# Kernel tuning notes

Measured on AMD Instinct MI355X. Metric: run time of the kernel, lower is better.

The kernel has to match this reference:

```python
import jax, jax.numpy as jnp
import numpy as np

H = 16  # head_num


def setup_inputs() -> dict:
    key = jax.random.key(0)
    ks = jax.random.split(key, 16)
    B, N, D, DR = 4, 512, 1024, 128
    dk = D // H
    nrm = lambda i, shp, sc=1.0: jax.random.normal(ks[i], shp, jnp.float32) * sc
    inp = {
        "q": nrm(0, (B, N, D)),
        "k": nrm(1, (B, N, D)),
        "v": nrm(2, (B, N, D)),
        "r_k": nrm(3, (B, N, N, DR), 0.1),
        "r_v": nrm(4, (B, N, N, DR), 0.1),
        # learned params (Linear stored as [in, out] so y = x @ W + b)
        "Wq": nrm(5, (D, D), 1.0 / np.sqrt(D)), "bq": jnp.zeros((D,), jnp.float32),
        "Wk": nrm(6, (D, D), 1.0 / np.sqrt(D)), "bk": jnp.zeros((D,), jnp.float32),
        "Wv": nrm(7, (D, D), 1.0 / np.sqrt(D)), "bv": jnp.zeros((D,), jnp.float32),
        "Wrk": nrm(8, (DR, dk), 1.0 / np.sqrt(DR)), "brk": jnp.zeros((dk,), jnp.float32),
        "Wrv": nrm(9, (DR, dk), 1.0 / np.sqrt(DR)), "brv": jnp.zeros((dk,), jnp.float32),
        "Wo": nrm(10, (D, D), 1.0 / np.sqrt(D)), "bo": jnp.zeros((D,), jnp.float32),
    }
    return inp


def reference(q, k, v, r_k, r_v, Wq, bq, Wk, bk, Wv, bv, Wrk, brk, Wrv, brv, Wo, bo):
    B, N, D = q.shape
    dk = D // H
    scale = 1.0 / np.sqrt(dk).astype(np.float32)
    # relation projections ('concat' mode, rel_share=False): [B,N,N,d_rel] -> [B,N,N,d_k]
    rk = r_k @ Wrk + brk
    rv = r_v @ Wrv + brv

    def heads(x, W, b):  # [B,N,D] -> [B,H,N,dk]
        return (x @ W + b).reshape(B, N, H, dk).transpose(0, 2, 1, 3)

    qh = heads(q, Wq, bq)
    kh = heads(k, Wk, bk)
    vh = heads(v, Wv, bv)
    # score_1: standard scaled dot-product; score_2: relation bias per (query m, key n)
    score = jnp.einsum('bhmd,bhnd->bhmn', qh, kh) * scale \
          + jnp.einsum('bhmd,bmnd->bhmn', qh, rk)
    att = jax.nn.softmax(score, axis=-1)  # [B,H,N,N]
    # value_1: standard AV; value_2: relation-value combination
    val = jnp.einsum('bhmn,bhnd->bhmd', att, vh) \
        + jnp.einsum('bhmn,bmnd->bhmd', att, rv)
    out = val.transpose(0, 2, 1, 3).reshape(B, N, D) @ Wo + bo
    return out
```

## Files before the change

### kernel.cpp

```cpp
#include <hip/hip_runtime.h>
#include <hip/hip_bf16.h>
#include <hip/hip_fp16.h>
#include <stdint.h>


typedef __attribute__((ext_vector_type(4))) float f32x4;
typedef __attribute__((ext_vector_type(8))) short s16x8;

#define MFMA16(A, B, C) __builtin_amdgcn_mfma_f32_16x16x32_bf16(A, B, C, 0, 0, 0)

__device__ __forceinline__ uint16_t f2bf(float x) {
  uint32_t u = __float_as_uint(x);
  u += 0x7fffu + ((u >> 16) & 1u);
  return (uint16_t)(u >> 16);
}
__device__ __forceinline__ float bf2f(uint16_t u) {
  return __uint_as_float((uint32_t)u << 16);
}
__device__ __forceinline__ uint16_t f2h(float x) {
  __half h = __float2half_rn(x);
  return *reinterpret_cast<uint16_t*>(&h);
}
__device__ __forceinline__ float h2f(uint16_t u) {
  __half h = *reinterpret_cast<__half*>(&u);
  return __half2float(h);
}

__device__ __forceinline__ s16x8 pack8(float4 a, float4 b) {
  s16x8 r;
  r[0] = (short)f2bf(a.x); r[1] = (short)f2bf(a.y); r[2] = (short)f2bf(a.z); r[3] = (short)f2bf(a.w);
  r[4] = (short)f2bf(b.x); r[5] = (short)f2bf(b.y); r[6] = (short)f2bf(b.z); r[7] = (short)f2bf(b.w);
  return r;
}

__device__ __forceinline__ void gll16(const void* g, void* l) {
  __builtin_amdgcn_global_load_lds(
      (const __attribute__((address_space(1))) uint32_t*)(g),
      (__attribute__((address_space(3))) uint32_t*)(l), 16, 0, 0);
}

__global__ __launch_bounds__(256) void k_prep(
    const float* __restrict__ Wq, const float* __restrict__ Wk,
    const float* __restrict__ Wv, const float* __restrict__ Wo,
    const float* __restrict__ Wrk, const float* __restrict__ Wrv,
    uint16_t* __restrict__ WqT, uint16_t* __restrict__ WkT,
    uint16_t* __restrict__ WvT, uint16_t* __restrict__ WoT,
    uint16_t* __restrict__ WrkB, uint16_t* __restrict__ WrvT) {
  int z = blockIdx.y;
  int t = threadIdx.x;
  if (z == 4) {
    if (blockIdx.x == 0) {
      for (int i = t; i < 128 * 64; i += 256) WrkB[i] = f2bf(Wrk[i]);
      for (int i = t; i < 64 * 128; i += 256) {
        int d = i >> 7, r = i & 127;
        WrvT[i] = f2bf(Wrv[r * 64 + d]);
      }
    }
    return;
  }
  const float* W = (z == 0) ? Wq : (z == 1) ? Wk : (z == 2) ? Wv : Wo;
  uint16_t* O = (z == 0) ? WqT : (z == 1) ? WkT : (z == 2) ? WvT : WoT;
  int tk = (blockIdx.x >> 4) * 64;
  int tn = (blockIdx.x & 15) * 64;
  __shared__ float tile[64][65];
  {
    int kk = t >> 2, c0 = (t & 3) * 16;
    const float* src = W + (size_t)(tk + kk) * 1024 + tn + c0;
#pragma unroll
    for (int i = 0; i < 16; i += 4) {
      float4 v = *(const float4*)(src + i);
      tile[kk][c0 + i + 0] = v.x; tile[kk][c0 + i + 1] = v.y;
      tile[kk][c0 + i + 2] = v.z; tile[kk][c0 + i + 3] = v.w;
    }
  }
  __syncthreads();
  {
    int n_loc = t >> 2;
    int n = tn + n_loc;
#pragma unroll
    for (int cc = 0; cc < 2; ++cc) {
      int c = (t & 3) * 2 + cc;
      int csrc = c ^ (n & 7);
      s16x8 pk;
#pragma unroll
      for (int j = 0; j < 8; ++j) pk[j] = (short)f2bf(tile[csrc * 8 + j][n_loc]);
      *reinterpret_cast<s16x8*>(O + (size_t)n * 1024 + tk + c * 8) = pk;
    }
  }
}

__global__ __launch_bounds__(256) void k_projqkv(
    const float* __restrict__ Xq, const float* __restrict__ Xk,
    const float* __restrict__ Xv, const uint16_t* __restrict__ WTbase,
    const float* __restrict__ bq, const float* __restrict__ bk,
    const float* __restrict__ bv, uint16_t* __restrict__ outbase) {
  int mode = blockIdx.z;
  const float* X = (mode == 0) ? Xq : (mode == 1) ? Xk : Xv;
  const float* bias = (mode == 0) ? bq : (mode == 1) ? bk : bv;
  const uint16_t* WT = WTbase + (size_t)mode * (1u << 20);
  uint16_t* out = outbase + (size_t)mode * (2u << 20);

  __shared__ alignas(16) uint16_t As[128 * 64];
  __shared__ alignas(16) uint16_t Bs[128 * 64];
  int t = threadIdx.x, lane = t & 63, w = t >> 6, lr = lane & 15, lg = lane >> 4;
  int m0 = blockIdx.x * 128, n0 = blockIdx.y * 128;
  int wm = (w >> 1) * 64, wn = (w & 1) * 64;
  f32x4 acc[4][4];
#pragma unroll
  for (int i = 0; i < 4; ++i)
#pragma unroll
    for (int j = 0; j < 4; ++j) acc[i][j] = (f32x4){0.f, 0.f, 0.f, 0.f};
  int srow = t >> 1, sh = t & 1;
  for (int ko = 0; ko < 16; ++ko) {
    __syncthreads();
    {
      const float* src = X + (size_t)(m0 + srow) * 1024 + ko * 64 + sh * 32;
#pragma unroll
      for (int c = 0; c < 4; ++c) {
        float4 v0 = *(const float4*)(src + c * 8);
        float4 v1 = *(const float4*)(src + c * 8 + 4);
        s16x8 pk = pack8(v0, v1);
        *reinterpret_cast<s16x8*>((char*)As + srow * 128 +
                                  ((((sh * 4 + c) * 16)) ^ ((srow & 7) << 4))) = pk;
      }
      const uint16_t* bsrc = WT + (size_t)(n0 + srow) * 1024 + ko * 64 + sh * 32;
#pragma unroll
      for (int c = 0; c < 4; ++c) {
        s16x8 vb = *(const s16x8*)(bsrc + c * 8);
        *reinterpret_cast<s16x8*>((char*)Bs + srow * 128 + (sh * 4 + c) * 16) = vb;
      }
    }
    __syncthreads();
#pragma unroll
    for (int kk = 0; kk < 2; ++kk) {
      s16x8 af[4], bf[4];
#pragma unroll
      for (int mt = 0; mt < 4; ++mt) {
        int row = wm + mt * 16 + lr;
        af[mt] = *(const s16x8*)((const char*)As + row * 128 +
                                 (((kk * 32 + lg * 8) * 2) ^ ((row & 7) << 4)));
      }
#pragma unroll
      for (int nt = 0; nt < 4; ++nt) {
        int row = wn + nt * 16 + lr;
        bf[nt] = *(const s16x8*)((const char*)Bs + row * 128 +
                                 (((kk * 32 + lg * 8) * 2) ^ ((row & 7) << 4)));
      }
#pragma unroll
      for (int mt = 0; mt < 4; ++mt)
#pragma unroll
        for (int nt = 0; nt < 4; ++nt)
          acc[mt][nt] = MFMA16(af[mt], bf[nt], acc[mt][nt]);
    }
  }
  float sc = (mode == 1) ? 0.125f : 1.0f;
#pragma unroll
  for (int mt = 0; mt < 4; ++mt) {
#pragma unroll
    for (int nt = 0; nt < 4; ++nt) {
      int col = n0 + wn + nt * 16 + lr;
      float bcol = bias[col];
      if (mode != 2) {
#pragma unroll
        for (int r = 0; r < 4; ++r) {
          int row = m0 + wm + mt * 16 + lg * 4 + r;
          out[(size_t)row * 1024 + col] = f2bf((acc[mt][nt][r] + bcol) * sc);
        }
      } else {
        int row0 = m0 + wm + mt * 16 + lg * 4;
        int b = row0 >> 9, n = row0 & 511;
        int h = col >> 6, d = col & 63;
        ushort4 pk;
        pk.x = f2bf(acc[mt][nt][0] + bcol);
        pk.y = f2bf(acc[mt][nt][1] + bcol);
        pk.z = f2bf(acc[mt][nt][2] + bcol);
        pk.w = f2bf(acc[mt][nt][3] + bcol);
        *reinterpret_cast<ushort4*>(out + ((size_t)(b * 16 + h) * 64 + d) * 512 + n) = pk;
      }
    }
  }
}

__global__ __launch_bounds__(256) void k_qt(
    const uint16_t* __restrict__ qh, const uint16_t* __restrict__ WrkB,
    uint16_t* __restrict__ qt) {
  int t = threadIdx.x, lane = t & 63, w = t >> 6, lr = lane & 15, lg = lane >> 4;
  int row0 = blockIdx.x * 64 + w * 16;
  f32x4 acc[8];
#pragma unroll
  for (int i = 0; i < 8; ++i) acc[i] = (f32x4){0.f, 0.f, 0.f, 0.f};
  s16x8 af[2];
#pragma unroll
  for (int kk = 0; kk < 2; ++kk)
    af[kk] = *(const s16x8*)(qh + (size_t)(row0 + lr) * 64 + kk * 32 + lg * 8);
#pragma unroll
  for (int rt = 0; rt < 8; ++rt) {
#pragma unroll
    for (int kk = 0; kk < 2; ++kk) {
      s16x8 bf = *(const s16x8*)(WrkB + (size_t)(rt * 16 + lr) * 64 + kk * 32 + lg * 8);
      acc[rt] = MFMA16(af[kk], bf, acc[rt]);
    }
  }
#pragma unroll
  for (int rt = 0; rt < 8; ++rt)
#pragma unroll
    for (int r = 0; r < 4; ++r)
      qt[(size_t)(row0 + lg * 4 + r) * 128 + rt * 16 + lr] = f2bf(acc[rt][r]);
}

__global__ __launch_bounds__(256, 2) void k_score1(
    const uint16_t* __restrict__ qh, const uint16_t* __restrict__ kh,
    uint16_t* __restrict__ S1) {
  int t = threadIdx.x, lane = t & 63, w = t >> 6, lr = lane & 15, lg = lane >> 4;
  int mt = blockIdx.x, h = blockIdx.y, b = blockIdx.z;
  int mrow = b * 512 + mt * 64 + w * 16 + lr;
  const uint16_t* qrow = qh + (size_t)mrow * 1024 + h * 64 + lg * 8;
  s16x8 bq0 = *(const s16x8*)(qrow);
  s16x8 bq1 = *(const s16x8*)(qrow + 32);
  const uint16_t* krow = kh + ((size_t)b * 512 + lr) * 1024 + h * 64 + lg * 8;
  f32x4 acc[32];
#pragma unroll
  for (int i = 0; i < 32; ++i) acc[i] = (f32x4){0.f, 0.f, 0.f, 0.f};
#pragma unroll
  for (int g = 0; g < 4; ++g) {
    s16x8 ka[8][2];
#pragma unroll
    for (int i = 0; i < 8; ++i) {
      const uint16_t* p = krow + (size_t)((g * 8 + i) * 16) * 1024;
      ka[i][0] = *(const s16x8*)(p);
      ka[i][1] = *(const s16x8*)(p + 32);
    }
#pragma unroll
    for (int i = 0; i < 8; ++i) {
      acc[g * 8 + i] = MFMA16(ka[i][0], bq0, acc[g * 8 + i]);
      acc[g * 8 + i] = MFMA16(ka[i][1], bq1, acc[g * 8 + i]);
    }
  }
#pragma unroll
  for (int nt = 0; nt < 32; ++nt) {
    int nsw = (nt * 16 + lg * 4) ^ ((h & 7) << 3);
    ushort4 u;
    u.x = f2h(acc[nt][0]); u.y = f2h(acc[nt][1]);
    u.z = f2h(acc[nt][2]); u.w = f2h(acc[nt][3]);
    *(ushort4*)(S1 + (size_t)mrow * 8192 + h * 512 + nsw) = u;
  }
}

#define RKSTEP(s)                                                              \
  {                                                                            \
    asm volatile("s_waitcnt vmcnt(%0)" ::                                      \
                 "i"(((s) <= 27) ? 6 : (31 - (s)) * 2) : "memory");            \
    const char* bp_ = wpriv + ((s) & 3) * 2048 + lr * 128;                     \
    float4 v0_ = *(const float4*)(bp_ + (((lg * 2 + 0) ^ (lr & 7)) * 16));     \
    float4 v1_ = *(const float4*)(bp_ + (((lg * 2 + 1) ^ (lr & 7)) * 16));     \
    acc[(s) >> 2] = MFMA16(aqt[(s) & 3], pack8(v0_, v1_), acc[(s) >> 2]);      \
    if ((s) + 4 < 32) {                                                        \
      const int s2_ = (s) + 4;                                                 \
      const char* src_ = rkb + (size_t)((s2_ >> 2) * 64 + w * 16 + r_lo) * 512 \
                         + (s2_ & 3) * 128 + c16s * 16;                        \
      char* dst_ = wpriv + (s2_ & 3) * 2048 + lane * 16;                       \
      gll16(src_, dst_);                                                       \
      gll16(src_ + 8 * 512, dst_ + 1024);                                      \
    }                                                                          \
  }

__global__ __launch_bounds__(256, 3) void k_s2v2(
    const uint16_t* __restrict__ qt, const float* __restrict__ rk,
    const float* __restrict__ rv, uint16_t* SATT,
    const uint16_t* __restrict__ WrvT, const float* __restrict__ brv,
    uint16_t* __restrict__ V2) {
  int bm = blockIdx.x;
  int t = threadIdx.x, lane = t & 63, w = t >> 6, lr = lane & 15, lg = lane >> 4;
  __shared__ alignas(16) char stream_lds[32768];
  __shared__ alignas(16) uint16_t att_lds[16 * 512];
  __shared__ alignas(16) uint16_t arv_lds[16 * 128];
  __shared__ float red[2][16][4];
  char* wpriv = stream_lds + w * 8192;
  const int r_lo = lane >> 3;
  const int c16s = (lane & 7) ^ r_lo;

  s16x8 aqt[4];
#pragma unroll
  for (int kk = 0; kk < 4; ++kk)
    aqt[kk] = *(const s16x8*)(qt + ((size_t)bm * 16 + lr) * 128 + kk * 32 + lg * 8);
  const char* s1g = (const char*)(SATT + (size_t)bm * 8192);
#pragma unroll
  for (int i = 0; i < 4; ++i)
    gll16(s1g + i * 4096 + t * 16, (char*)att_lds + i * 4096 + t * 16);
  asm volatile("s_waitcnt vmcnt(0)" ::: "memory");

  const char* rkb = (const char*)(rk + (size_t)bm * 65536);
#pragma unroll
  for (int s2 = 0; s2 < 4; ++s2) {
    const char* src_ = rkb + (size_t)((s2 >> 2) * 64 + w * 16 + r_lo) * 512 +
                       (s2 & 3) * 128 + c16s * 16;
    char* dst_ = wpriv + (s2 & 3) * 2048 + lane * 16;
    gll16(src_, dst_);
    gll16(src_ + 8 * 512, dst_ + 1024);
  }

  f32x4 acc[8];
#pragma unroll
  for (int j = 0; j < 8; ++j) acc[j] = (f32x4){0.f, 0.f, 0.f, 0.f};

  RKSTEP(0)  RKSTEP(1)  RKSTEP(2)  RKSTEP(3)  RKSTEP(4)  RKSTEP(5)  RKSTEP(6)  RKSTEP(7)
  RKSTEP(8)  RKSTEP(9)  RKSTEP(10) RKSTEP(11) RKSTEP(12) RKSTEP(13) RKSTEP(14) RKSTEP(15)
  RKSTEP(16) RKSTEP(17) RKSTEP(18) RKSTEP(19) RKSTEP(20) RKSTEP(21) RKSTEP(22) RKSTEP(23)
  RKSTEP(24) RKSTEP(25) RKSTEP(26) RKSTEP(27) RKSTEP(28) RKSTEP(29) RKSTEP(30) RKSTEP(31)

  const char* rvb = (const char*)(rv + (size_t)bm * 65536);
#pragma unroll
  for (int c = 0; c < 2; ++c) {
#pragma unroll
    for (int g = 0; g < 4; ++g) {
      const char* src_ = rvb + (size_t)(c * 32 + g * 8 + r_lo) * 512 + w * 128 +
                         (lane & 7) * 16;
      gll16(src_, wpriv + c * 4096 + g * 1024 + lane * 16);
    }
  }
  __syncthreads();

#pragma unroll
  for (int idx = 0; idx < 8; ++idx) {
#pragma unroll
    for (int r = 0; r < 4; ++r) {
      int h = lg * 4 + r;
      int n = idx * 64 + w * 16 + lr;
      uint16_t s1v = *(const uint16_t*)((const char*)att_lds + h * 1024 +
                     (((uint32_t)n * 2) ^ ((uint32_t)(h & 7) << 4)));
      acc[idx][r] += h2f(s1v);
    }
  }

  float mrow[4], inv[4];
#pragma unroll
  for (int r = 0; r < 4; ++r) {
    float mx = acc[0][r];
#pragma unroll
    for (int j = 1; j < 8; ++j) mx = fmaxf(mx, acc[j][r]);
#pragma unroll
    for (int off = 1; off < 16; off <<= 1) mx = fmaxf(mx, __shfl_xor(mx, off, 64));
    mrow[r] = mx;
  }
  if (lr == 0) {
#pragma unroll
    for (int r = 0; r < 4; ++r) red[0][lg * 4 + r][w] = mrow[r];
  }
  __syncthreads();
#pragma unroll
  for (int r = 0; r < 4; ++r) {
    const float* p = red[0][lg * 4 + r];
    mrow[r] = fmaxf(fmaxf(p[0], p[1]), fmaxf(p[2], p[3]));
  }
#pragma unroll
  for (int r = 0; r < 4; ++r) {
    float s = 0.f;
#pragma unroll
    for (int j = 0; j < 8; ++j) {
      float pj = __expf(acc[j][r] - mrow[r]);
      acc[j][r] = pj;
      s += pj;
    }
#pragma unroll
    for (int off = 1; off < 16; off <<= 1) s += __shfl_xor(s, off, 64);
    inv[r] = s;
  }
  if (lr == 0) {
#pragma unroll
    for (int r = 0; r < 4; ++r) red[1][lg * 4 + r][w] = inv[r];
  }
  __syncthreads();
#pragma unroll
  for (int r = 0; r < 4; ++r) {
    const float* p = red[1][lg * 4 + r];
    inv[r] = 1.f / (p[0] + p[1] + p[2] + p[3]);
  }
#pragma unroll
  for (int r = 0; r < 4; ++r) {
    int h = lg * 4 + r;
#pragma unroll
    for (int idx = 0; idx < 8; ++idx) {
      int n = idx * 64 + w * 16 + lr;
      uint32_t off = (uint32_t)h * 1024 + (((uint32_t)n * 2) ^ ((uint32_t)(h & 7) << 4));
      *(uint16_t*)((char*)att_lds + off) = f2bf(acc[idx][r] * inv[r]);
    }
  }
  __syncthreads();

#pragma unroll
  for (int i = 0; i < 4; ++i) {
    s16x8 vv = *(const s16x8*)((const char*)att_lds + i * 4096 + t * 16);
    *(s16x8*)((char*)SATT + (size_t)bm * 16384 + i * 4096 + t * 16) = vv;
  }
  asm volatile("" ::: "memory");

  f32x4 arv0 = (f32x4){0.f, 0.f, 0.f, 0.f}, arv1 = arv0;
#define RV_CONSUME(c)                                                          \
  {                                                                            \
    s16x8 a_ = *(const s16x8*)((const char*)att_lds + lr * 1024 +              \
               (((uint32_t)((c) * 64 + lg * 16)) ^ ((uint32_t)(lr & 7) << 4)));\
    const float* vb_ = (const float*)(wpriv + ((c) & 1) * 4096);               \
    s16x8 bf0_, bf1_;                                                          \
    _Pragma("unroll")                                                          \
    for (int i = 0; i < 8; ++i) bf0_[i] = (short)f2bf(vb_[(lg * 8 + i) * 32 + lr]); \
    _Pragma("unroll")                                                          \
    for (int i = 0; i < 8; ++i) bf1_[i] = (short)f2bf(vb_[(lg * 8 + i) * 32 + 16 + lr]); \
    arv0 = MFMA16(a_, bf0_, arv0);                                             \
    arv1 = MFMA16(a_, bf1_, arv1);                                             \
  }
#pragma unroll 1
  for (int c = 0; c < 14; ++c) {
    asm volatile("s_waitcnt vmcnt(4)" ::: "memory");
    RV_CONSUME(c)
#pragma unroll
    for (int g = 0; g < 4; ++g) {
      const char* src_ = rvb + (size_t)((c + 2) * 32 + g * 8 + r_lo) * 512 + w * 128 +
                         (lane & 7) * 16;
      gll16(src_, wpriv + ((c + 2) & 1) * 4096 + g * 1024 + lane * 16);
    }
  }
  asm volatile("s_waitcnt vmcnt(4)" ::: "memory");
  RV_CONSUME(14)
  asm volatile("s_waitcnt vmcnt(0)" ::: "memory");
  RV_CONSUME(15)

#pragma unroll
  for (int r = 0; r < 4; ++r) {
    int h = lg * 4 + r;
    uint32_t rc0 = (uint32_t)(w * 32 + lr) * 2;
    uint32_t rc1 = (uint32_t)(w * 32 + 16 + lr) * 2;
    *(uint16_t*)((char*)arv_lds + h * 256 + (rc0 ^ ((uint32_t)(h & 7) << 4))) = f2bf(arv0[r]);
    *(uint16_t*)((char*)arv_lds + h * 256 + (rc1 ^ ((uint32_t)(h & 7) << 4))) = f2bf(arv1[r]);
  }
  __syncthreads();
  f32x4 vacc = (f32x4){0.f, 0.f, 0.f, 0.f};
#pragma unroll
  for (int kk = 0; kk < 4; ++kk) {
    uint32_t rb = (uint32_t)(kk * 32 + lg * 8) * 2;
    s16x8 a = *(const s16x8*)((const char*)arv_lds + lr * 256 +
                              (rb ^ ((uint32_t)(lr & 7) << 4)));
    s16x8 bfw = *(const s16x8*)(WrvT + (size_t)(w * 16 + lr) * 128 + kk * 32 + lg * 8);
    vacc = MFMA16(a, bfw, vacc);
  }
  float bias = brv[w * 16 + lr];
#pragma unroll
  for (int r = 0; r < 4; ++r)
    V2[(size_t)bm * 1024 + (lg * 4 + r) * 64 + w * 16 + lr] = f2bf(vacc[r] + bias);
}

__global__ __launch_bounds__(256) void k_val1(
    const uint16_t* __restrict__ vhT, const uint16_t* __restrict__ ATT,
    const uint16_t* __restrict__ V2, uint16_t* __restrict__ VALB) {
  int t = threadIdx.x, lane = t & 63, w = t >> 6, lr = lane & 15, lg = lane >> 4;
  int mt = blockIdx.x, h = blockIdx.y, b = blockIdx.z;
  int mb = mt * 64 + w * 16;
  const uint16_t* vrow = vhT + ((size_t)((b * 16 + h) * 64) + lr) * 512 + lg * 8;
  const uint16_t* arow = ATT + (size_t)(b * 512 + mb + lr) * 8192 + h * 512;
  f32x4 acc[4];
#pragma unroll
  for (int j = 0; j < 4; ++j) acc[j] = (f32x4){0.f, 0.f, 0.f, 0.f};
#pragma unroll 4
  for (int kk = 0; kk < 16; ++kk) {
    int nsw = (kk * 32 + lg * 8) ^ ((h & 7) << 3);
    s16x8 a0 = *(const s16x8*)(arow + nsw);
#pragma unroll
    for (int dt = 0; dt < 4; ++dt) {
      s16x8 vf = *(const s16x8*)(vrow + (size_t)dt * 16 * 512 + kk * 32);
      acc[dt] = MFMA16(vf, a0, acc[dt]);
    }
  }
#pragma unroll
  for (int dt = 0; dt < 4; ++dt) {
    size_t adr = (size_t)(b * 512 + mb + lr) * 1024 + h * 64 + dt * 16 + lg * 4;
    ushort4 v2v = *(const ushort4*)(V2 + adr);
    ushort4 o;
    o.x = f2bf(acc[dt][0] + bf2f(v2v.x));
    o.y = f2bf(acc[dt][1] + bf2f(v2v.y));
    o.z = f2bf(acc[dt][2] + bf2f(v2v.z));
    o.w = f2bf(acc[dt][3] + bf2f(v2v.w));
    *(ushort4*)(VALB + adr) = o;
  }
}

__global__ __launch_bounds__(256) void k_out(
    const uint16_t* __restrict__ A, const uint16_t* __restrict__ WT,
    const float* __restrict__ bias, float* __restrict__ out) {
  __shared__ alignas(16) uint16_t As[128 * 64];
  __shared__ alignas(16) uint16_t Bs[128 * 64];
  int t = threadIdx.x, lane = t & 63, w = t >> 6, lr = lane & 15, lg = lane >> 4;
  int m0 = blockIdx.x * 128, n0 = blockIdx.y * 128;
  int wm = (w >> 1) * 64, wn = (w & 1) * 64;
  f32x4 acc[4][4];
#pragma unroll
  for (int i = 0; i < 4; ++i)
#pragma unroll
    for (int j = 0; j < 4; ++j) acc[i][j] = (f32x4){0.f, 0.f, 0.f, 0.f};
  int srow = t >> 1, sh = t & 1;
  for (int ko = 0; ko < 16; ++ko) {
    __syncthreads();
    {
      const uint16_t* asrc = A + (size_t)(m0 + srow) * 1024 + ko * 64 + sh * 32;
      const uint16_t* bsrc = WT + (size_t)(n0 + srow) * 1024 + ko * 64 + sh * 32;
#pragma unroll
      for (int c = 0; c < 4; ++c) {
        s16x8 va = *(const s16x8*)(asrc + c * 8);
        *reinterpret_cast<s16x8*>((char*)As + srow * 128 +
                                  ((((sh * 4 + c) * 16)) ^ ((srow & 7) << 4))) = va;
        s16x8 vb = *(const s16x8*)(bsrc + c * 8);
        *reinterpret_cast<s16x8*>((char*)Bs + srow * 128 + (sh * 4 + c) * 16) = vb;
      }
    }
    __syncthreads();
#pragma unroll
    for (int kk = 0; kk < 2; ++kk) {
      s16x8 af[4], bf[4];
#pragma unroll
      for (int mt = 0; mt < 4; ++mt) {
        int row = wm + mt * 16 + lr;
        af[mt] = *(const s16x8*)((const char*)As + row * 128 +
                                 (((kk * 32 + lg * 8) * 2) ^ ((row & 7) << 4)));
      }
#pragma unroll
      for (int nt = 0; nt < 4; ++nt) {
        int row = wn + nt * 16 + lr;
        bf[nt] = *(const s16x8*)((const char*)Bs + row * 128 +
                                 (((kk * 32 + lg * 8) * 2) ^ ((row & 7) << 4)));
      }
#pragma unroll
      for (int mt = 0; mt < 4; ++mt)
#pragma unroll
        for (int nt = 0; nt < 4; ++nt)
          acc[mt][nt] = MFMA16(af[mt], bf[nt], acc[mt][nt]);
    }
  }
#pragma unroll
  for (int mt = 0; mt < 4; ++mt) {
#pragma unroll
    for (int nt = 0; nt < 4; ++nt) {
      int col = n0 + wn + nt * 16 + lr;
      float bcol = bias[col];
#pragma unroll
      for (int r = 0; r < 4; ++r) {
        int row = m0 + wm + mt * 16 + lg * 4 + r;
        out[(size_t)row * 1024 + col] = acc[mt][nt][r] + bcol;
      }
    }
  }
}

extern "C" void kernel_launch(void* const* d_in, const int* in_sizes, int n_in,
                              void* d_out, int out_size, void* d_ws, size_t ws_size,
                              hipStream_t stream) {
  const float* q   = (const float*)d_in[0];
  const float* k_  = (const float*)d_in[1];
  const float* v   = (const float*)d_in[2];
  const float* r_k = (const float*)d_in[3];
  const float* r_v = (const float*)d_in[4];
  const float* Wq  = (const float*)d_in[5];
  const float* bq  = (const float*)d_in[6];
  const float* Wk  = (const float*)d_in[7];
  const float* bk  = (const float*)d_in[8];
  const float* Wv  = (const float*)d_in[9];
  const float* bv  = (const float*)d_in[10];
  const float* Wrk = (const float*)d_in[11];
  const float* Wrv = (const float*)d_in[13];
  const float* brv = (const float*)d_in[14];
  const float* Wo  = (const float*)d_in[15];
  const float* bo  = (const float*)d_in[16];
  (void)in_sizes; (void)n_in; (void)out_size;

  char* ws = (char*)d_ws;
  uint16_t* WqT  = (uint16_t*)(ws + (size_t)(0));
  uint16_t* WkT  = (uint16_t*)(ws + (size_t)(2u << 20));
  uint16_t* WvT  = (uint16_t*)(ws + (size_t)(4u << 20));
  uint16_t* WoT  = (uint16_t*)(ws + (size_t)(6u << 20));
  uint16_t* WrkB = (uint16_t*)(ws + (size_t)(8u << 20));
  uint16_t* WrvT = (uint16_t*)(ws + (size_t)(8u << 20) + (64u << 10));
  uint16_t* QH   = (uint16_t*)(ws + (size_t)(16u << 20));
  uint16_t* KH   = (uint16_t*)(ws + (size_t)(20u << 20));
  uint16_t* VHT  = (uint16_t*)(ws + (size_t)(24u << 20));
  uint16_t* QT   = (uint16_t*)(ws + (size_t)(28u << 20));
  uint16_t* VALB = (uint16_t*)(ws + (size_t)(36u << 20));
  uint16_t* V2   = (uint16_t*)(ws + (size_t)(16u << 20));
  uint16_t* SATT = (uint16_t*)(ws + (size_t)(40u << 20));
  if (ws_size < (size_t)(74u << 20)) return;

  dim3 blk(256, 1, 1);
  k_prep<<<dim3(256, 5, 1), blk, 0, stream>>>(Wq, Wk, Wv, Wo, Wrk, Wrv,
                                              WqT, WkT, WvT, WoT, WrkB, WrvT);
  k_projqkv<<<dim3(16, 8, 3), blk, 0, stream>>>(q, k_, v, WqT, bq, bk, bv, QH);
  k_qt<<<dim3(512, 1, 1), blk, 0, stream>>>(QH, WrkB, QT);
  k_score1<<<dim3(8, 16, 4), blk, 0, stream>>>(QH, KH, SATT);
  k_s2v2<<<dim3(2048, 1, 1), blk, 0, stream>>>(QT, r_k, r_v, SATT, WrvT, brv, V2);
  k_val1<<<dim3(8, 16, 4), blk, 0, stream>>>(VHT, SATT, V2, VALB);
  k_out<<<dim3(16, 8, 1), blk, 0, stream>>>(VALB, WoT, bo, (float*)d_out);
}
```

Measured before the change: 380.0 us.

## Rework score1 tiling, shrink s2v2 LDS pipeline, split val1 and async-load weights

Several independent changes land together. The weight tiles in the projection and output GEMMs now load asynchronously straight into LDS. k_score1 becomes a 128x128 LDS-tiled MFMA GEMM. k_s2v2 shrinks its per-wave streaming buffers to double-buffering so it can run 4 blocks per CU, restructures the r_v loop, and moves the attention writeback to the end of the kernel. k_val1 splits the head dimension across twice as many blocks. The aim is lower load latency and higher occupancy in the bandwidth-bound relation kernel, at the cost of a shallower prefetch depth, which may expose memory latency.

```diff
diff --git a/kernel.cpp b/kernel.cpp
--- a/kernel.cpp
+++ b/kernel.cpp
@@ -114,6 +114,12 @@
   for (int ko = 0; ko < 16; ++ko) {
     __syncthreads();
     {
+#pragma unroll
+      for (int i = 0; i < 4; ++i) {
+        int u = i * 256 + t;
+        int row = u >> 3, c2 = u & 7;
+        gll16(WT + (size_t)(n0 + row) * 1024 + ko * 64 + c2 * 8, (char*)Bs + u * 16);
+      }
       const float* src = X + (size_t)(m0 + srow) * 1024 + ko * 64 + sh * 32;
 #pragma unroll
       for (int c = 0; c < 4; ++c) {
@@ -122,12 +128,6 @@
         s16x8 pk = pack8(v0, v1);
         *reinterpret_cast<s16x8*>((char*)As + srow * 128 +
                                   ((((sh * 4 + c) * 16)) ^ ((srow & 7) << 4))) = pk;
-      }
-      const uint16_t* bsrc = WT + (size_t)(n0 + srow) * 1024 + ko * 64 + sh * 32;
-#pragma unroll
-      for (int c = 0; c < 4; ++c) {
-        s16x8 vb = *(const s16x8*)(bsrc + c * 8);
-        *reinterpret_cast<s16x8*>((char*)Bs + srow * 128 + (sh * 4 + c) * 16) = vb;
       }
     }
     __syncthreads();
@@ -208,74 +208,116 @@
       qt[(size_t)(row0 + lg * 4 + r) * 128 + rt * 16 + lr] = f2bf(acc[rt][r]);
 }
 
-__global__ __launch_bounds__(256, 2) void k_score1(
+__global__ __launch_bounds__(256) void k_score1(
     const uint16_t* __restrict__ qh, const uint16_t* __restrict__ kh,
     uint16_t* __restrict__ S1) {
+  __shared__ alignas(16) uint16_t As[128 * 64];
+  __shared__ alignas(16) uint16_t Bs[128 * 64];
   int t = threadIdx.x, lane = t & 63, w = t >> 6, lr = lane & 15, lg = lane >> 4;
-  int mt = blockIdx.x, h = blockIdx.y, b = blockIdx.z;
-  int mrow = b * 512 + mt * 64 + w * 16 + lr;
-  const uint16_t* qrow = qh + (size_t)mrow * 1024 + h * 64 + lg * 8;
-  s16x8 bq0 = *(const s16x8*)(qrow);
-  s16x8 bq1 = *(const s16x8*)(qrow + 32);
-  const uint16_t* krow = kh + ((size_t)b * 512 + lr) * 1024 + h * 64 + lg * 8;
-  f32x4 acc[32];
-#pragma unroll
-  for (int i = 0; i < 32; ++i) acc[i] = (f32x4){0.f, 0.f, 0.f, 0.f};
-#pragma unroll
-  for (int g = 0; g < 4; ++g) {
-    s16x8 ka[8][2];
-#pragma unroll
-    for (int i = 0; i < 8; ++i) {
-      const uint16_t* p = krow + (size_t)((g * 8 + i) * 16) * 1024;
-      ka[i][0] = *(const s16x8*)(p);
-      ka[i][1] = *(const s16x8*)(p + 32);
-    }
-#pragma unroll
-    for (int i = 0; i < 8; ++i) {
-      acc[g * 8 + i] = MFMA16(ka[i][0], bq0, acc[g * 8 + i]);
-      acc[g * 8 + i] = MFMA16(ka[i][1], bq1, acc[g * 8 + i]);
-    }
-  }
-#pragma unroll
-  for (int nt = 0; nt < 32; ++nt) {
-    int nsw = (nt * 16 + lg * 4) ^ ((h & 7) << 3);
-    ushort4 u;
-    u.x = f2h(acc[nt][0]); u.y = f2h(acc[nt][1]);
-    u.z = f2h(acc[nt][2]); u.w = f2h(acc[nt][3]);
-    *(ushort4*)(S1 + (size_t)mrow * 8192 + h * 512 + nsw) = u;
+  int mt = blockIdx.x >> 2, nt = blockIdx.x & 3, h = blockIdx.y, b = blockIdx.z;
+  int m0 = mt * 128, n0 = nt * 128;
+  const char* qg = (const char*)(qh + (size_t)(b * 512 + m0) * 1024 + h * 64);
+  const char* kg = (const char*)(kh + (size_t)(b * 512 + n0) * 1024 + h * 64);
+#pragma unroll
+  for (int i = 0; i < 4; ++i) {
+    int u = i * 256 + t;
+    int row = u >> 3;
+    int cs = (u & 7) ^ (row & 7);
+    gll16(qg + (size_t)row * 2048 + cs * 16, (char*)As + u * 16);
+    gll16(kg + (size_t)row * 2048 + cs * 16, (char*)Bs + u * 16);
+  }
+  __syncthreads();
+  int wm = (w >> 1) * 64, wn = (w & 1) * 64;
+  f32x4 acc[4][4];
+#pragma unroll
+  for (int i = 0; i < 4; ++i)
+#pragma unroll
+    for (int j = 0; j < 4; ++j) acc[i][j] = (f32x4){0.f, 0.f, 0.f, 0.f};
+#pragma unroll
+  for (int kk = 0; kk < 2; ++kk) {
+    s16x8 af[4], bf[4];
+#pragma unroll
+    for (int mtt = 0; mtt < 4; ++mtt) {
+      int row = wm + mtt * 16 + lr;
+      af[mtt] = *(const s16x8*)((const char*)As + row * 128 +
+                                (((kk * 4 + lg) ^ (row & 7)) * 16));
+    }
+#pragma unroll
+    for (int ntt = 0; ntt < 4; ++ntt) {
+      int row = wn + ntt * 16 + lr;
+      bf[ntt] = *(const s16x8*)((const char*)Bs + row * 128 +
+                                (((kk * 4 + lg) ^ (row & 7)) * 16));
+    }
+#pragma unroll
+    for (int mtt = 0; mtt < 4; ++mtt)
+#pragma unroll
+      for (int ntt = 0; ntt < 4; ++ntt)
+        acc[mtt][ntt] = MFMA16(bf[ntt], af[mtt], acc[mtt][ntt]);
+  }
+  int hsw = (h & 7) << 3;
+#pragma unroll
+  for (int mtt = 0; mtt < 4; ++mtt) {
+#pragma unroll
+    for (int ntt = 0; ntt < 4; ++ntt) {
+      int m = b * 512 + m0 + wm + mtt * 16 + lr;
+      int nsw = (n0 + wn + ntt * 16 + lg * 4) ^ hsw;
+      ushort4 u4;
+      u4.x = f2h(acc[mtt][ntt][0]); u4.y = f2h(acc[mtt][ntt][1]);
+      u4.z = f2h(acc[mtt][ntt][2]); u4.w = f2h(acc[mtt][ntt][3]);
+      *(ushort4*)(S1 + (size_t)m * 8192 + h * 512 + nsw) = u4;
+    }
   }
 }
 
 #define RKSTEP(s)                                                              \
   {                                                                            \
-    asm volatile("s_waitcnt vmcnt(%0)" ::                                      \
-                 "i"(((s) <= 27) ? 6 : (31 - (s)) * 2) : "memory");            \
-    const char* bp_ = wpriv + ((s) & 3) * 2048 + lr * 128;                     \
+    asm volatile("s_waitcnt vmcnt(%0)" :: "i"(((s) < 31) ? 2 : 0) : "memory"); \
+    const char* bp_ = wpriv + ((s) & 1) * 2048 + lr * 128;                     \
     float4 v0_ = *(const float4*)(bp_ + (((lg * 2 + 0) ^ (lr & 7)) * 16));     \
     float4 v1_ = *(const float4*)(bp_ + (((lg * 2 + 1) ^ (lr & 7)) * 16));     \
     acc[(s) >> 2] = MFMA16(aqt[(s) & 3], pack8(v0_, v1_), acc[(s) >> 2]);      \
-    if ((s) + 4 < 32) {                                                        \
-      const int s2_ = (s) + 4;                                                 \
+    if ((s) + 2 < 32) {                                                        \
+      const int s2_ = (s) + 2;                                                 \
       const char* src_ = rkb + (size_t)((s2_ >> 2) * 64 + w * 16 + r_lo) * 512 \
                          + (s2_ & 3) * 128 + c16s * 16;                        \
-      char* dst_ = wpriv + (s2_ & 3) * 2048 + lane * 16;                       \
+      char* dst_ = wpriv + (s2_ & 1) * 2048 + lane * 16;                       \
       gll16(src_, dst_);                                                       \
       gll16(src_ + 8 * 512, dst_ + 1024);                                      \
     }                                                                          \
   }
 
-__global__ __launch_bounds__(256, 3) void k_s2v2(
+#define RVI(c)                                                                 \
+  { _Pragma("unroll")                                                          \
+    for (int i_ = 0; i_ < 2; ++i_) {                                           \
+      int u_ = i_ * 64 + lane;                                                 \
+      gll16(rvb + (size_t)(((c) >> 1) * 32 + (u_ >> 2)) * 512 + w * 128 +      \
+                ((c) & 1) * 64 + (u_ & 3) * 16,                                \
+            wpriv + ((c) & 1) * 2048 + u_ * 16);                               \
+    } }
+
+#define RVC(c, accv)                                                           \
+  {                                                                            \
+    s16x8 a_ = *(const s16x8*)((const char*)att_lds + lr * 1024 +              \
+        (((uint32_t)(((c) >> 1) * 64 + lg * 16)) ^ ((uint32_t)(lr & 7) << 4)));\
+    const float* vb_ = (const float*)(wpriv + ((c) & 1) * 2048);               \
+    s16x8 bf_;                                                                 \
+    _Pragma("unroll")                                                          \
+    for (int i = 0; i < 8; ++i) bf_[i] = (short)f2bf(vb_[(lg * 8 + i) * 16 + lr]); \
+    accv = MFMA16(a_, bf_, accv);                                              \
+  }
+
+__global__ __launch_bounds__(256, 4) void k_s2v2(
     const uint16_t* __restrict__ qt, const float* __restrict__ rk,
     const float* __restrict__ rv, uint16_t* SATT,
     const uint16_t* __restrict__ WrvT, const float* __restrict__ brv,
     uint16_t* __restrict__ V2) {
   int bm = blockIdx.x;
   int t = threadIdx.x, lane = t & 63, w = t >> 6, lr = lane & 15, lg = lane >> 4;
-  __shared__ alignas(16) char stream_lds[32768];
+  __shared__ alignas(16) char stream_lds[16384];
   __shared__ alignas(16) uint16_t att_lds[16 * 512];
   __shared__ alignas(16) uint16_t arv_lds[16 * 128];
   __shared__ float red[2][16][4];
-  char* wpriv = stream_lds + w * 8192;
+  char* wpriv = stream_lds + w * 4096;
   const int r_lo = lane >> 3;
   const int c16s = (lane & 7) ^ r_lo;
 
@@ -291,10 +333,9 @@
 
   const char* rkb = (const char*)(rk + (size_t)bm * 65536);
 #pragma unroll
-  for (int s2 = 0; s2 < 4; ++s2) {
-    const char* src_ = rkb + (size_t)((s2 >> 2) * 64 + w * 16 + r_lo) * 512 +
-                       (s2 & 3) * 128 + c16s * 16;
-    char* dst_ = wpriv + (s2 & 3) * 2048 + lane * 16;
+  for (int s2 = 0; s2 < 2; ++s2) {
+    const char* src_ = rkb + (size_t)(w * 16 + r_lo) * 512 + s2 * 128 + c16s * 16;
+    char* dst_ = wpriv + s2 * 2048 + lane * 16;
     gll16(src_, dst_);
     gll16(src_ + 8 * 512, dst_ + 1024);
   }
@@ -309,15 +350,7 @@
   RKSTEP(24) RKSTEP(25) RKSTEP(26) RKSTEP(27) RKSTEP(28) RKSTEP(29) RKSTEP(30) RKSTEP(31)
 
   const char* rvb = (const char*)(rv + (size_t)bm * 65536);
-#pragma unroll
-  for (int c = 0; c < 2; ++c) {
-#pragma unroll
-    for (int g = 0; g < 4; ++g) {
-      const char* src_ = rvb + (size_t)(c * 32 + g * 8 + r_lo) * 512 + w * 128 +
-                         (lane & 7) * 16;
-      gll16(src_, wpriv + c * 4096 + g * 1024 + lane * 16);
-    }
-  }
+  RVI(0) RVI(1)
   __syncthreads();
 
 #pragma unroll
@@ -387,42 +420,26 @@
   }
   __syncthreads();
 
-#pragma unroll
-  for (int i = 0; i < 4; ++i) {
-    s16x8 vv = *(const s16x8*)((const char*)att_lds + i * 4096 + t * 16);
-    *(s16x8*)((char*)SATT + (size_t)bm * 16384 + i * 4096 + t * 16) = vv;
-  }
-  asm volatile("" ::: "memory");
-
   f32x4 arv0 = (f32x4){0.f, 0.f, 0.f, 0.f}, arv1 = arv0;
-#define RV_CONSUME(c)                                                          \
-  {                                                                            \
-    s16x8 a_ = *(const s16x8*)((const char*)att_lds + lr * 1024 +              \
-               (((uint32_t)((c) * 64 + lg * 16)) ^ ((uint32_t)(lr & 7) << 4)));\
-    const float* vb_ = (const float*)(wpriv + ((c) & 1) * 4096);               \
-    s16x8 bf0_, bf1_;                                                          \
-    _Pragma("unroll")                                                          \
-    for (int i = 0; i < 8; ++i) bf0_[i] = (short)f2bf(vb_[(lg * 8 + i) * 32 + lr]); \
-    _Pragma("unroll")                                                          \
-    for (int i = 0; i < 8; ++i) bf1_[i] = (short)f2bf(vb_[(lg * 8 + i) * 32 + 16 + lr]); \
-    arv0 = MFMA16(a_, bf0_, arv0);                                             \
-    arv1 = MFMA16(a_, bf1_, arv1);                                             \
-  }
 #pragma unroll 1
-  for (int c = 0; c < 14; ++c) {
-    asm volatile("s_waitcnt vmcnt(4)" ::: "memory");
-    RV_CONSUME(c)
-#pragma unroll
-    for (int g = 0; g < 4; ++g) {
-      const char* src_ = rvb + (size_t)((c + 2) * 32 + g * 8 + r_lo) * 512 + w * 128 +
-                         (lane & 7) * 16;
-      gll16(src_, wpriv + ((c + 2) & 1) * 4096 + g * 1024 + lane * 16);
-    }
-  }
-  asm volatile("s_waitcnt vmcnt(4)" ::: "memory");
-  RV_CONSUME(14)
+  for (int cp = 0; cp < 14; ++cp) {
+    asm volatile("s_waitcnt vmcnt(2)" ::: "memory");
+    RVC(2 * cp, arv0)
+    RVI(2 * cp + 2)
+    asm volatile("s_waitcnt vmcnt(2)" ::: "memory");
+    RVC(2 * cp + 1, arv1)
+    RVI(2 * cp + 3)
+  }
+  asm volatile("s_waitcnt vmcnt(2)" ::: "memory");
+  RVC(28, arv0)
+  RVI(30)
+  asm volatile("s_waitcnt vmcnt(2)" ::: "memory");
+  RVC(29, arv1)
+  RVI(31)
+  asm volatile("s_waitcnt vmcnt(2)" ::: "memory");
+  RVC(30, arv0)
   asm volatile("s_waitcnt vmcnt(0)" ::: "memory");
-  RV_CONSUME(15)
+  RVC(31, arv1)
 
 #pragma unroll
   for (int r = 0; r < 4; ++r) {
@@ -446,32 +463,38 @@
 #pragma unroll
   for (int r = 0; r < 4; ++r)
     V2[(size_t)bm * 1024 + (lg * 4 + r) * 64 + w * 16 + lr] = f2bf(vacc[r] + bias);
+
+#pragma unroll
+  for (int i = 0; i < 4; ++i) {
+    s16x8 vv = *(const s16x8*)((const char*)att_lds + i * 4096 + t * 16);
+    *(s16x8*)((char*)SATT + (size_t)bm * 16384 + i * 4096 + t * 16) = vv;
+  }
 }
 
 __global__ __launch_bounds__(256) void k_val1(
     const uint16_t* __restrict__ vhT, const uint16_t* __restrict__ ATT,
     const uint16_t* __restrict__ V2, uint16_t* __restrict__ VALB) {
   int t = threadIdx.x, lane = t & 63, w = t >> 6, lr = lane & 15, lg = lane >> 4;
-  int mt = blockIdx.x, h = blockIdx.y, b = blockIdx.z;
+  int mt = blockIdx.x >> 1, dh = blockIdx.x & 1, h = blockIdx.y, b = blockIdx.z;
   int mb = mt * 64 + w * 16;
-  const uint16_t* vrow = vhT + ((size_t)((b * 16 + h) * 64) + lr) * 512 + lg * 8;
+  const uint16_t* vrow = vhT + ((size_t)((b * 16 + h) * 64) + dh * 32 + lr) * 512 + lg * 8;
   const uint16_t* arow = ATT + (size_t)(b * 512 + mb + lr) * 8192 + h * 512;
-  f32x4 acc[4];
-#pragma unroll
-  for (int j = 0; j < 4; ++j) acc[j] = (f32x4){0.f, 0.f, 0.f, 0.f};
+  f32x4 acc[2];
+#pragma unroll
+  for (int j = 0; j < 2; ++j) acc[j] = (f32x4){0.f, 0.f, 0.f, 0.f};
 #pragma unroll 4
   for (int kk = 0; kk < 16; ++kk) {
     int nsw = (kk * 32 + lg * 8) ^ ((h & 7) << 3);
     s16x8 a0 = *(const s16x8*)(arow + nsw);
 #pragma unroll
-    for (int dt = 0; dt < 4; ++dt) {
+    for (int dt = 0; dt < 2; ++dt) {
       s16x8 vf = *(const s16x8*)(vrow + (size_t)dt * 16 * 512 + kk * 32);
       acc[dt] = MFMA16(vf, a0, acc[dt]);
     }
   }
 #pragma unroll
-  for (int dt = 0; dt < 4; ++dt) {
-    size_t adr = (size_t)(b * 512 + mb + lr) * 1024 + h * 64 + dt * 16 + lg * 4;
+  for (int dt = 0; dt < 2; ++dt) {
+    size_t adr = (size_t)(b * 512 + mb + lr) * 1024 + h * 64 + dh * 32 + dt * 16 + lg * 4;
     ushort4 v2v = *(const ushort4*)(V2 + adr);
     ushort4 o;
     o.x = f2bf(acc[dt][0] + bf2f(v2v.x));
@@ -499,15 +522,18 @@
   for (int ko = 0; ko < 16; ++ko) {
     __syncthreads();
     {
+#pragma unroll
+      for (int i = 0; i < 4; ++i) {
+        int u = i * 256 + t;
+        int row = u >> 3, c2 = u & 7;
+        gll16(WT + (size_t)(n0 + row) * 1024 + ko * 64 + c2 * 8, (char*)Bs + u * 16);
+      }
       const uint16_t* asrc = A + (size_t)(m0 + srow) * 1024 + ko * 64 + sh * 32;
-      const uint16_t* bsrc = WT + (size_t)(n0 + srow) * 1024 + ko * 64 + sh * 32;
 #pragma unroll
       for (int c = 0; c < 4; ++c) {
         s16x8 va = *(const s16x8*)(asrc + c * 8);
         *reinterpret_cast<s16x8*>((char*)As + srow * 128 +
                                   ((((sh * 4 + c) * 16)) ^ ((srow & 7) << 4))) = va;
-        s16x8 vb = *(const s16x8*)(bsrc + c * 8);
-        *reinterpret_cast<s16x8*>((char*)Bs + srow * 128 + (sh * 4 + c) * 16) = vb;
       }
     }
     __syncthreads();
@@ -590,8 +616,8 @@
                                               WqT, WkT, WvT, WoT, WrkB, WrvT);
   k_projqkv<<<dim3(16, 8, 3), blk, 0, stream>>>(q, k_, v, WqT, bq, bk, bv, QH);
   k_qt<<<dim3(512, 1, 1), blk, 0, stream>>>(QH, WrkB, QT);
-  k_score1<<<dim3(8, 16, 4), blk, 0, stream>>>(QH, KH, SATT);
+  k_score1<<<dim3(16, 16, 4), blk, 0, stream>>>(QH, KH, SATT);
   k_s2v2<<<dim3(2048, 1, 1), blk, 0, stream>>>(QT, r_k, r_v, SATT, WrvT, brv, V2);
-  k_val1<<<dim3(8, 16, 4), blk, 0, stream>>>(VHT, SATT, V2, VALB);
+  k_val1<<<dim3(16, 16, 4), blk, 0, stream>>>(VHT, SATT, V2, VALB);
   k_out<<<dim3(16, 8, 1), blk, 0, stream>>>(VALB, WoT, bo, (float*)d_out);
 }
```

New measurement: 382.4 us. No clear change (+0.6%).
